# Optimization experiments

Hardware: AMD Instinct MI355X
Metric: run time of the kernel (lower is better)

The kernel has to match this reference:

```python
import jax, jax.numpy as jnp
import numpy as np

B, S, D, H = 2, 2048, 1024, 16
HD = D // H  # head_dim = 64


def setup_inputs() -> dict:
    key = jax.random.key(0)
    ks = jax.random.split(key, 6)
    scale = 0.02
    return {
        "x": jax.random.normal(ks[0], (B, S, D), dtype=jnp.float32),
        "wq": jax.random.normal(ks[1], (D, D), dtype=jnp.float32) * scale,  # torch Linear weight [out,in]
        "wk": jax.random.normal(ks[2], (D, D), dtype=jnp.float32) * scale,
        "wv": jax.random.normal(ks[3], (D, D), dtype=jnp.float32) * scale,
        "wo": jax.random.normal(ks[4], (D, D), dtype=jnp.float32) * scale,
        "bo": jnp.zeros((D,), dtype=jnp.float32),
    }


def reference(x, wq, wk, wv, wo, bo):
    b, t, d = x.shape
    # projections (torch nn.Linear: x @ W.T), split into heads -> [b, h, t, hd]
    def split_heads(y):
        return y.reshape(b, t, H, HD).transpose(0, 2, 1, 3)

    q = split_heads(x @ wq.T)
    k = split_heads(x @ wk.T)
    v = split_heads(x @ wv.T)

    scores = jnp.einsum("bhqd,bhkd->bhqk", q, k)  # [b,h,t,t]
    causal = jnp.triu(jnp.ones((t, t), dtype=bool), k=1)
    scores = jnp.where(causal, -jnp.inf, scores)
    attn = jax.nn.softmax(scores / jnp.sqrt(jnp.asarray(HD, scores.dtype)), axis=-1)
    # dropout p=0.0 -> identity (eval-mode reference)
    ctx = jnp.einsum("bhqk,bhkd->bhqd", attn, v)
    ctx = ctx.transpose(0, 2, 1, 3).reshape(b, t, d)
    return ctx @ wo.T + bo
```

## Files before the change

kernel.cpp:

```cpp
#include <hip/hip_runtime.h>
#include <hip/hip_bf16.h>
#include <stdint.h>
#include <math.h>

#define NH   16
#define HDIM 64
#define SEQ  2048
#define DM   1024
#define NB   2
#define MTOK (NB * SEQ)

typedef __bf16 bf16x8 __attribute__((ext_vector_type(8)));
typedef __bf16 bf16x4 __attribute__((ext_vector_type(4)));
typedef short  short4v __attribute__((ext_vector_type(4)));
typedef float  f32x4  __attribute__((ext_vector_type(4)));

__device__ __forceinline__ unsigned short f2bf(float f) {
  union { float f; unsigned int u; } c; c.f = f;
  unsigned int u = c.u;
  return (unsigned short)((u + 0x7FFFu + ((u >> 16) & 1u)) >> 16);
}
__device__ __forceinline__ float bf2f(unsigned short s) {
  union { unsigned int u; float f; } c; c.u = ((unsigned int)s) << 16;
  return c.f;
}
__device__ __forceinline__ unsigned int pk2bf(float a, float b) {
  __hip_bfloat162 h = __float22bfloat162_rn(float2{a, b});
  return *reinterpret_cast<unsigned int*>(&h);
}

__device__ __forceinline__ f32x4 mfma16(short4v a, short4v b, f32x4 c) {
#if __has_builtin(__builtin_amdgcn_mfma_f32_16x16x16_bf16)
  return __builtin_amdgcn_mfma_f32_16x16x16_bf16(
      __builtin_bit_cast(bf16x4, a), __builtin_bit_cast(bf16x4, b), c, 0, 0, 0);
#else
  return __builtin_amdgcn_mfma_f32_16x16x16bf16_1k(a, b, c, 0, 0, 0);
#endif
}

__device__ __forceinline__ void async_copy16(const void* g, void* l) {
  __builtin_amdgcn_global_load_lds((__attribute__((address_space(1))) void*)g,
                                   (__attribute__((address_space(3))) void*)l,
                                   16, 0, 0);
}

__global__ void cast_all(const float* __restrict__ x,  const float* __restrict__ wq,
                         const float* __restrict__ wk, const float* __restrict__ wv,
                         const float* __restrict__ wo,
                         unsigned short* __restrict__ xb,
                         unsigned short* __restrict__ wqkvb,
                         unsigned short* __restrict__ wob) {
  const int i = blockIdx.x * 256 + threadIdx.x;
  float4 v;
  uint2* dstp;
  int idx;
  if (i < (1 << 20)) {
    v = reinterpret_cast<const float4*>(x)[i];
    dstp = reinterpret_cast<uint2*>(xb); idx = i;
  } else {
    const int j = i - (1 << 20);
    const int seg = j >> 18;
    idx = j & ((1 << 18) - 1);
    const float* w = (seg == 0) ? wq : (seg == 1) ? wk : (seg == 2) ? wv : wo;
    v = reinterpret_cast<const float4*>(w)[idx];
    if (seg < 3) { dstp = reinterpret_cast<uint2*>(wqkvb); idx += seg * (1 << 18); }
    else         { dstp = reinterpret_cast<uint2*>(wob); }
  }
  uint2 o;
  o.x = pk2bf(v.x, v.y); o.y = pk2bf(v.z, v.w);
  dstp[idx] = o;
}

#define QSCALE 0.1803368801111244f
template <int MODE>
__global__ __launch_bounds__(256, 3) void gemm_bt(
    const unsigned short* __restrict__ A,
    const unsigned short* __restrict__ B,
    unsigned short* __restrict__ qo, unsigned short* __restrict__ ko,
    unsigned short* __restrict__ vo,
    float* __restrict__ co, const float* __restrict__ bias,
    int M, int N, int K) {
  constexpr int BN = (MODE == 0) ? 128 : 64;
  constexpr int TJ = BN / 32;
  constexpr int RB = BN * 4 / 256;
  __shared__ __align__(16) unsigned short As[128 * 32];
  __shared__ __align__(16) unsigned short Bs[BN * 32];

  const int tid  = threadIdx.x;
  const int lane = tid & 63;
  const int wave = tid >> 6;
  const int l15  = lane & 15;
  const int quad = lane >> 4;
  const int wm   = (wave >> 1) * 64;
  const int wn   = (wave & 1) * (BN / 2);
  const int m0   = blockIdx.x * 128;
  const int n0   = blockIdx.y * BN;

  f32x4 acc[4][TJ];
#pragma unroll
  for (int a = 0; a < 4; ++a)
#pragma unroll
    for (int b = 0; b < TJ; ++b) acc[a][b] = f32x4{0.f, 0.f, 0.f, 0.f};

  for (int k0 = 0; k0 < K; k0 += 32) {
    __syncthreads();
#pragma unroll
    for (int s = 0; s < 2; ++s) {
      const int c   = tid + s * 256;
      const int row = c >> 2;
      const int col = (c & 3) * 8;
      unsigned short* lA = As + ((size_t)wave * 64 + s * 256) * 8;
      async_copy16(A + (size_t)(m0 + row) * K + k0 + col, lA);
    }
#pragma unroll
    for (int s = 0; s < RB; ++s) {
      const int c   = tid + s * 256;
      const int row = c >> 2;
      const int col = (c & 3) * 8;
      unsigned short* lB = Bs + ((size_t)wave * 64 + s * 256) * 8;
      async_copy16(B + (size_t)(n0 + row) * K + k0 + col, lB);
    }
    __syncthreads();

    bf16x8 af[4], bfr[TJ];
#pragma unroll
    for (int t = 0; t < 4; ++t)
      af[t]  = *reinterpret_cast<const bf16x8*>(As + (wm + t * 16 + l15) * 32 + quad * 8);
#pragma unroll
    for (int t = 0; t < TJ; ++t)
      bfr[t] = *reinterpret_cast<const bf16x8*>(Bs + (wn + t * 16 + l15) * 32 + quad * 8);
#pragma unroll
    for (int ti = 0; ti < 4; ++ti)
#pragma unroll
      for (int tj = 0; tj < TJ; ++tj)
        acc[ti][tj] = __builtin_amdgcn_mfma_f32_16x16x32_bf16(af[ti], bfr[tj], acc[ti][tj], 0, 0, 0);
  }

#pragma unroll
  for (int ti = 0; ti < 4; ++ti) {
#pragma unroll
    for (int tj = 0; tj < TJ; ++tj) {
      const int mb = m0 + wm + ti * 16 + quad * 4;
      const int n  = n0 + wn + tj * 16 + l15;
      if (MODE == 0) {
        const int which = n >> 10;
        const int n1 = n & 1023;
        const int h = n1 >> 6, d = n1 & 63;
        const int b = mb >> 11, s = mb & 2047;
        if (which == 0) {
          const size_t idx = ((size_t)(b * NH + h) * SEQ + s) * HDIM + d;
#pragma unroll
          for (int r = 0; r < 4; ++r) qo[idx + (size_t)r * HDIM] = f2bf(acc[ti][tj][r] * QSCALE);
        } else if (which == 1) {
          const size_t idx = ((size_t)(b * NH + h) * SEQ + s) * HDIM + d;
#pragma unroll
          for (int r = 0; r < 4; ++r) ko[idx + (size_t)r * HDIM] = f2bf(acc[ti][tj][r]);
        } else {
          const size_t idx = ((size_t)(b * NH + h) * HDIM + d) * SEQ + s;
          uint2 pk;
          pk.x = pk2bf(acc[ti][tj][0], acc[ti][tj][1]);
          pk.y = pk2bf(acc[ti][tj][2], acc[ti][tj][3]);
          *reinterpret_cast<uint2*>(vo + idx) = pk;
        }
      } else {
#pragma unroll
        for (int r = 0; r < 4; ++r)
          co[(size_t)(mb + r) * N + n] = acc[ti][tj][r] + bias[n];
      }
    }
  }
}

__global__ __launch_bounds__(256, 5) void flash_attn_mfma(
    const unsigned short* __restrict__ Qb,
    const unsigned short* __restrict__ Kb,
    const unsigned short* __restrict__ Vtg,
    unsigned short* __restrict__ ctx,
    unsigned short* __restrict__ pO,
    float* __restrict__ pL) {
  __shared__ __align__(16) unsigned short Ks[2][64 * 64];
  __shared__ __align__(16) unsigned short Vt[2][64 * 64];

  const int tid  = threadIdx.x;
  const int bh   = blockIdx.y;
  const int lane = tid & 63;
  const int wave = tid >> 6;
  const int l15  = lane & 15;
  const int quad = lane >> 4;
  const int sw   = l15 & 7;

  int qt, chunk, nch;
  {
    const int x = blockIdx.x;
    if (x < 12)      { qt = x;                 chunk = 0;            nch = 1; }
    else if (x < 36) { qt = 12 + (x - 12) / 2; chunk = (x - 12) % 2; nch = 2; }
    else             { qt = 24 + (x - 36) / 3; chunk = (x - 36) % 3; nch = 3; }
  }
  const int q0 = qt * 64;
  const int c0 = chunk * 12;
  const int c1 = min(qt, c0 + 11);

  const size_t baseQK = (size_t)bh * SEQ * HDIM;
  const size_t baseV  = (size_t)bh * HDIM * SEQ;

  const unsigned short* kptr[2];
  const unsigned short* vptr[2];
  unsigned short* ldst = nullptr;
  int ldsc[2];
#pragma unroll
  for (int s = 0; s < 2; ++s) {
    const int P   = s * 256 + tid;
    const int row = P >> 3;
    const int cc  = ((P & 7) ^ (row & 7)) * 8;
    kptr[s] = Kb + baseQK + (size_t)(c0 * 64 + row) * HDIM + cc;
    vptr[s] = Vtg + baseV + (size_t)row * SEQ + c0 * 64 + cc;
    ldsc[s] = (s * 256 + wave * 64) * 8;
  }
  (void)ldst;

  bf16x8 qf[2];
  {
    const unsigned short* qp = Qb + baseQK + (size_t)(q0 + wave * 16 + l15) * HDIM + quad * 8;
    qf[0] = *reinterpret_cast<const bf16x8*>(qp);
    qf[1] = *reinterpret_cast<const bf16x8*>(qp + 32);
  }

  float l_acc = 0.f;
  f32x4 o[4];
#pragma unroll
  for (int td = 0; td < 4; ++td) o[td] = f32x4{0.f, 0.f, 0.f, 0.f};

#pragma unroll
  for (int s = 0; s < 2; ++s) {
    async_copy16(kptr[s], &Ks[0][ldsc[s]]);
    async_copy16(vptr[s], &Vt[0][ldsc[s]]);
    kptr[s] += 64 * HDIM;
    vptr[s] += 64;
  }

  for (int kt = c0; kt <= c1; ++kt) {
    const int buf = (kt - c0) & 1;
    __syncthreads();

    if (kt < c1) {
#pragma unroll
      for (int s = 0; s < 2; ++s) {
        async_copy16(kptr[s], &Ks[buf ^ 1][ldsc[s]]);
        async_copy16(vptr[s], &Vt[buf ^ 1][ldsc[s]]);
        kptr[s] += 64 * HDIM;
        vptr[s] += 64;
      }
    }

    const int tmax = (kt == qt) ? wave : 3;

#pragma unroll
    for (int t = 0; t < 4; ++t) {
      if (t <= tmax) {
        f32x4 c = f32x4{0.f, 0.f, 0.f, 0.f};
        const int krow = (t * 16 + l15) * 64;
        const bf16x8 kf0 = *reinterpret_cast<const bf16x8*>(&Ks[buf][krow + (quad ^ sw) * 8]);
        const bf16x8 kf1 = *reinterpret_cast<const bf16x8*>(&Ks[buf][krow + ((4 + quad) ^ sw) * 8]);
        c = __builtin_amdgcn_mfma_f32_16x16x32_bf16(kf0, qf[0], c, 0, 0, 0);
        c = __builtin_amdgcn_mfma_f32_16x16x32_bf16(kf1, qf[1], c, 0, 0, 0);
        if (kt == qt && t == wave) {
#pragma unroll
          for (int r = 0; r < 4; ++r)
            if (quad * 4 + r > l15) c[r] = -INFINITY;
        }

        const float p0 = exp2f(c[0]);
        const float p1 = exp2f(c[1]);
        const float p2 = exp2f(c[2]);
        const float p3 = exp2f(c[3]);
        l_acc += (p0 + p1) + (p2 + p3);
        union { uint2 u; short4v s; } pf;
        pf.u.x = pk2bf(p0, p1);
        pf.u.y = pk2bf(p2, p3);

        const int lc = 2 * t + (quad >> 1);
        const int vcol = ((lc ^ sw) * 8) + (quad & 1) * 4;
#pragma unroll
        for (int td = 0; td < 4; ++td) {
          const short4v vf = *reinterpret_cast<const short4v*>(
              &Vt[buf][(td * 16 + l15) * 64 + vcol]);
          o[td] = mfma16(pf.s, vf, o[td]);
        }
      }
    }
  }

  float l_s = l_acc;
  l_s += __shfl_xor(l_s, 16, 64);
  l_s += __shfl_xor(l_s, 32, 64);

  if (nch == 1) {
    const float linv = 1.f / l_s;
    const int b = bh >> 4, h = bh & 15;
#pragma unroll
    for (int r = 0; r < 4; ++r) {
      const float lr = __shfl(linv, quad * 4 + r, 64);
      const int sr = q0 + wave * 16 + quad * 4 + r;
      const size_t ob = (size_t)(b * SEQ + sr) * DM + h * HDIM + l15;
#pragma unroll
      for (int td = 0; td < 4; ++td)
        ctx[ob + td * 16] = f2bf(o[td][r] * lr);
    }
  } else {
    const int pb = (qt < 24) ? 2 * (qt - 12) : 24 + 3 * (qt - 24);
    const int pidx = bh * 48 + pb + chunk;
    if (quad == 0) pL[pidx * 64 + wave * 16 + l15] = l_s;
    unsigned short* po = pO + (size_t)pidx * 4096;
#pragma unroll
    for (int r = 0; r < 4; ++r) {
      const int ql = wave * 16 + quad * 4 + r;
#pragma unroll
      for (int td = 0; td < 4; ++td)
        po[ql * 64 + td * 16 + l15] = f2bf(o[td][r]);
    }
  }
}

__global__ __launch_bounds__(256, 8) void attn_reduce(
    const unsigned short* __restrict__ pO, const float* __restrict__ pL,
    unsigned short* __restrict__ ctx) {
  const int x = blockIdx.x;
  int qt, pb, nch;
  if (x < 12) { qt = 12 + x; pb = 2 * x;            nch = 2; }
  else        { qt = 24 + (x - 12); pb = 24 + 3 * (x - 12); nch = 3; }
  const int bh = blockIdx.y;
  const int b = bh >> 4, h = bh & 15;
  const int pidx = bh * 48 + pb;

  const int tid = threadIdx.x;
  const int ql  = tid >> 2;
  const int d0  = (tid & 3) * 16;

  float acc[16];
#pragma unroll
  for (int e = 0; e < 16; ++e) acc[e] = 0.f;
  float lsum = 0.f;

  for (int c = 0; c < nch; ++c) {
    lsum += pL[(pidx + c) * 64 + ql];
    const unsigned short* src = pO + (size_t)(pidx + c) * 4096 + ql * 64 + d0;
    const uint4 v0 = *reinterpret_cast<const uint4*>(src);
    const uint4 v1 = *reinterpret_cast<const uint4*>(src + 8);
    const unsigned short* u = reinterpret_cast<const unsigned short*>(&v0);
    const unsigned short* w = reinterpret_cast<const unsigned short*>(&v1);
#pragma unroll
    for (int e = 0; e < 8; ++e) { acc[e] += bf2f(u[e]); acc[8 + e] += bf2f(w[e]); }
  }

  const float linv = 1.f / lsum;
  unsigned int outw[8];
#pragma unroll
  for (int e = 0; e < 8; ++e)
    outw[e] = pk2bf(acc[2 * e] * linv, acc[2 * e + 1] * linv);
  unsigned short* dst = ctx + (size_t)(b * SEQ + qt * 64 + ql) * DM + h * HDIM + d0;
  *reinterpret_cast<uint4*>(dst)     = *reinterpret_cast<uint4*>(&outw[0]);
  *reinterpret_cast<uint4*>(dst + 8) = *reinterpret_cast<uint4*>(&outw[4]);
}

extern "C" void kernel_launch(void* const* d_in, const int* in_sizes, int n_in,
                              void* d_out, int out_size, void* d_ws, size_t ws_size,
                              hipStream_t stream) {
  const float* x  = (const float*)d_in[0];
  const float* wq = (const float*)d_in[1];
  const float* wk = (const float*)d_in[2];
  const float* wv = (const float*)d_in[3];
  const float* wo = (const float*)d_in[4];
  const float* bo = (const float*)d_in[5];
  float* out = (float*)d_out;

  char* ws = (char*)d_ws;
  unsigned short* xb    = (unsigned short*)(ws);
  unsigned short* wqkvb = (unsigned short*)(ws + (8ull  << 20));
  unsigned short* wob   = (unsigned short*)(ws + (14ull << 20));
  unsigned short* Qb    = (unsigned short*)(ws + (16ull << 20));
  unsigned short* Kb    = (unsigned short*)(ws + (24ull << 20));
  unsigned short* Vtg   = (unsigned short*)(ws + (32ull << 20));
  unsigned short* ctxb  = (unsigned short*)(ws + (40ull << 20));
  unsigned short* pO    = (unsigned short*)(ws);
  float*          pL    = (float*)(ws + (12ull << 20));

  cast_all<<<8192, 256, 0, stream>>>(x, wq, wk, wv, wo, xb, wqkvb, wob);

  dim3 g1(MTOK / 128, (3 * DM) / 128);
  gemm_bt<0><<<g1, 256, 0, stream>>>(xb, wqkvb, Qb, Kb, Vtg, nullptr, nullptr,
                                     MTOK, 3 * DM, DM);

  dim3 g2(60, NB * NH);
  flash_attn_mfma<<<g2, 256, 0, stream>>>(Qb, Kb, Vtg, ctxb, pO, pL);

  dim3 gr(20, NB * NH);
  attn_reduce<<<gr, 256, 0, stream>>>(pO, pL, ctxb);

  dim3 g3(MTOK / 128, DM / 64);
  gemm_bt<1><<<g3, 256, 0, stream>>>(ctxb, wob, nullptr, nullptr, nullptr, out, bo,
                                     MTOK, DM, DM);
}
```

Baseline: 195.1 us.

## Single-buffer attention K/V tiles to raise occupancy, use raw exp2, retune launch bounds

The flash attention kernel drops its double-buffered K/V shared-memory tiles for a single buffer, loading each tile synchronously between two barriers, and raises the launch-bounds occupancy target from 5 to 8 blocks. The goal is to fit more resident blocks per CU so other waves hide the load latency, in place of explicit prefetch overlap. The exp2 calls become the hardware exp2 builtin, which skips the library's range handling. The GEMM launch bound drops from 3 to 2 blocks, giving the compiler more registers per thread. The risk is that load latency is no longer hidden inside a block, and the extra barrier per tile adds stalls.

```diff
diff --git a/kernel.cpp b/kernel.cpp
--- a/kernel.cpp
+++ b/kernel.cpp
@@ -27,6 +27,14 @@
 __device__ __forceinline__ unsigned int pk2bf(float a, float b) {
   __hip_bfloat162 h = __float22bfloat162_rn(float2{a, b});
   return *reinterpret_cast<unsigned int*>(&h);
+}
+
+__device__ __forceinline__ float fexp2(float x) {
+#if __has_builtin(__builtin_amdgcn_exp2f)
+  return __builtin_amdgcn_exp2f(x);
+#else
+  return exp2f(x);
+#endif
 }
 
 __device__ __forceinline__ f32x4 mfma16(short4v a, short4v b, f32x4 c) {
@@ -73,7 +81,7 @@
 
 #define QSCALE 0.1803368801111244f
 template <int MODE>
-__global__ __launch_bounds__(256, 3) void gemm_bt(
+__global__ __launch_bounds__(256, 2) void gemm_bt(
     const unsigned short* __restrict__ A,
     const unsigned short* __restrict__ B,
     unsigned short* __restrict__ qo, unsigned short* __restrict__ ko,
@@ -171,15 +179,15 @@
   }
 }
 
-__global__ __launch_bounds__(256, 5) void flash_attn_mfma(
+__global__ __launch_bounds__(256, 8) void flash_attn_mfma(
     const unsigned short* __restrict__ Qb,
     const unsigned short* __restrict__ Kb,
     const unsigned short* __restrict__ Vtg,
     unsigned short* __restrict__ ctx,
     unsigned short* __restrict__ pO,
     float* __restrict__ pL) {
-  __shared__ __align__(16) unsigned short Ks[2][64 * 64];
-  __shared__ __align__(16) unsigned short Vt[2][64 * 64];
+  __shared__ __align__(16) unsigned short Ks[64 * 64];
+  __shared__ __align__(16) unsigned short Vt[64 * 64];
 
   const int tid  = threadIdx.x;
   const int bh   = blockIdx.y;
@@ -205,7 +213,6 @@
 
   const unsigned short* kptr[2];
   const unsigned short* vptr[2];
-  unsigned short* ldst = nullptr;
   int ldsc[2];
 #pragma unroll
   for (int s = 0; s < 2; ++s) {
@@ -216,7 +223,6 @@
     vptr[s] = Vtg + baseV + (size_t)row * SEQ + c0 * 64 + cc;
     ldsc[s] = (s * 256 + wave * 64) * 8;
   }
-  (void)ldst;
 
   bf16x8 qf[2];
   {
@@ -230,27 +236,16 @@
 #pragma unroll
   for (int td = 0; td < 4; ++td) o[td] = f32x4{0.f, 0.f, 0.f, 0.f};
 
-#pragma unroll
-  for (int s = 0; s < 2; ++s) {
-    async_copy16(kptr[s], &Ks[0][ldsc[s]]);
-    async_copy16(vptr[s], &Vt[0][ldsc[s]]);
-    kptr[s] += 64 * HDIM;
-    vptr[s] += 64;
-  }
-
   for (int kt = c0; kt <= c1; ++kt) {
-    const int buf = (kt - c0) & 1;
     __syncthreads();
-
-    if (kt < c1) {
-#pragma unroll
-      for (int s = 0; s < 2; ++s) {
-        async_copy16(kptr[s], &Ks[buf ^ 1][ldsc[s]]);
-        async_copy16(vptr[s], &Vt[buf ^ 1][ldsc[s]]);
-        kptr[s] += 64 * HDIM;
-        vptr[s] += 64;
-      }
-    }
+#pragma unroll
+    for (int s = 0; s < 2; ++s) {
+      async_copy16(kptr[s], &Ks[ldsc[s]]);
+      async_copy16(vptr[s], &Vt[ldsc[s]]);
+      kptr[s] += 64 * HDIM;
+      vptr[s] += 64;
+    }
+    __syncthreads();
 
     const int tmax = (kt == qt) ? wave : 3;
 
@@ -259,8 +254,8 @@
       if (t <= tmax) {
         f32x4 c = f32x4{0.f, 0.f, 0.f, 0.f};
         const int krow = (t * 16 + l15) * 64;
-        const bf16x8 kf0 = *reinterpret_cast<const bf16x8*>(&Ks[buf][krow + (quad ^ sw) * 8]);
-        const bf16x8 kf1 = *reinterpret_cast<const bf16x8*>(&Ks[buf][krow + ((4 + quad) ^ sw) * 8]);
+        const bf16x8 kf0 = *reinterpret_cast<const bf16x8*>(&Ks[krow + (quad ^ sw) * 8]);
+        const bf16x8 kf1 = *reinterpret_cast<const bf16x8*>(&Ks[krow + ((4 + quad) ^ sw) * 8]);
         c = __builtin_amdgcn_mfma_f32_16x16x32_bf16(kf0, qf[0], c, 0, 0, 0);
         c = __builtin_amdgcn_mfma_f32_16x16x32_bf16(kf1, qf[1], c, 0, 0, 0);
         if (kt == qt && t == wave) {
@@ -269,10 +264,10 @@
             if (quad * 4 + r > l15) c[r] = -INFINITY;
         }
 
-        const float p0 = exp2f(c[0]);
-        const float p1 = exp2f(c[1]);
-        const float p2 = exp2f(c[2]);
-        const float p3 = exp2f(c[3]);
+        const float p0 = fexp2(c[0]);
+        const float p1 = fexp2(c[1]);
+        const float p2 = fexp2(c[2]);
+        const float p3 = fexp2(c[3]);
         l_acc += (p0 + p1) + (p2 + p3);
         union { uint2 u; short4v s; } pf;
         pf.u.x = pk2bf(p0, p1);
@@ -283,7 +278,7 @@
 #pragma unroll
         for (int td = 0; td < 4; ++td) {
           const short4v vf = *reinterpret_cast<const short4v*>(
-              &Vt[buf][(td * 16 + l15) * 64 + vcol]);
+              &Vt[(td * 16 + l15) * 64 + vcol]);
           o[td] = mfma16(pf.s, vf, o[td]);
         }
       }
```

New measurement: 186.2 us. 4.6% less time.
